# Optimization experiments

Measured on AMD Instinct MI355X. Metric: run time of the kernel, lower is better.

## Reference

```python
import jax, jax.numpy as jnp
import numpy as np

B, S, D, H = 4, 2048, 1024, 16
HD = D // H  # head_size = 64


def setup_inputs() -> dict:
    key = jax.random.key(0)
    kx, kq, kk, kv = jax.random.split(key, 4)
    scale = 1.0 / np.sqrt(D)
    return {
        "x": jax.random.normal(kx, (B, S, D), dtype=jnp.float32),
        "Wq": jax.random.normal(kq, (H, HD, D), dtype=jnp.float32) * scale,
        "Wk": jax.random.normal(kk, (H, HD, D), dtype=jnp.float32) * scale,
        "Wv": jax.random.normal(kv, (H, HD, D), dtype=jnp.float32) * scale,
    }


def reference(x, Wq, Wk, Wv):
    # Per-head projections (Linear with weight [out, in]: y = x @ W.T),
    # vectorized over heads: [B,S,D] x [H,HD,D] -> [B,H,S,HD]
    q = jnp.einsum('bsd,hed->bhse', x, Wq)
    k = jnp.einsum('bsd,hed->bhse', x, Wk)
    v = jnp.einsum('bsd,hed->bhse', x, Wv)

    # Scaled scores: [B,H,S,S]
    att = jnp.einsum('bhqe,bhke->bhqk', q, k) / jnp.sqrt(jnp.asarray(HD, x.dtype))

    # Causal mask (lower-triangular incl. diagonal)
    causal = jnp.tril(jnp.ones((S, S), dtype=bool))
    att = jnp.where(causal, att, -jnp.inf)
    att = jax.nn.softmax(att, axis=-1)

    # Weighted values, then concat heads along feature dim -> [B,S,D]
    out = jnp.einsum('bhqk,bhke->bhqe', att, v)
    out = out.transpose(0, 2, 1, 3).reshape(B, S, H * HD)
    return out
```

## Files before the change

kernel.cpp:

```cpp
#include <hip/hip_runtime.h>
#include <hip/hip_bf16.h>

#define BATCH 4
#define S_LEN 2048
#define D_DIM 1024
#define NHEAD 16
#define HDIM 64

#define QSCALE 0.18033688011112042f

typedef __attribute__((ext_vector_type(8))) __bf16 bf16x8;
typedef __attribute__((ext_vector_type(4))) __bf16 bf16x4;
typedef __attribute__((ext_vector_type(4))) float f32x4;
typedef __attribute__((ext_vector_type(16))) float f32x16;

static __device__ inline unsigned int bf16_bits(float f) {
    __bf16 h = (__bf16)f;
    return (unsigned int)__builtin_bit_cast(unsigned short, h);
}
static __device__ inline unsigned int pkbf(float a, float b) {
    return bf16_bits(a) | (bf16_bits(b) << 16);
}

#define NX8 1048576
#define NW8 131072

__global__ __launch_bounds__(256) void cvt_all_kernel(
    const float* __restrict__ x,  const float* __restrict__ Wq,
    const float* __restrict__ Wk, const float* __restrict__ Wv,
    __bf16* __restrict__ xb, __bf16* __restrict__ wcat)
{
    const int i = blockIdx.x * 256 + threadIdx.x;
    const float* src;
    __bf16* dst;
    if (i < NX8) {
        src = x + (size_t)i * 8;
        dst = xb + (size_t)i * 8;
    } else {
        const int i2 = i - NX8;
        const int w  = i2 >> 17;
        src = ((w == 0) ? Wq : (w == 1) ? Wk : Wv) + (size_t)(i2 & (NW8 - 1)) * 8;
        dst = wcat + (size_t)i2 * 8;
    }
    const f32x4* p = reinterpret_cast<const f32x4*>(src);
    f32x4 a = p[0], b = p[1];
    bf16x8 r;
    r[0] = (__bf16)a[0]; r[1] = (__bf16)a[1]; r[2] = (__bf16)a[2]; r[3] = (__bf16)a[3];
    r[4] = (__bf16)b[0]; r[5] = (__bf16)b[1]; r[6] = (__bf16)b[2]; r[7] = (__bf16)b[3];
    *reinterpret_cast<bf16x8*>(dst) = r;
}

__global__ __launch_bounds__(256) void proj_gemm_kernel(
    const __bf16* __restrict__ xb, const __bf16* __restrict__ wb,
    __bf16* __restrict__ qo, __bf16* __restrict__ ko, __bf16* __restrict__ vto)
{
    __shared__ __bf16 As[128][32];
    __shared__ __bf16 Bs[128][32];

    const int tid = threadIdx.x;
    const int l  = tid & 63;
    const int w  = tid >> 6;
    const int wm = w >> 1, wn = w & 1;
    const int lr = l & 15, lg = l >> 4, lk = lg * 8;
    const int m0 = blockIdx.y * 128;
    const int n0 = blockIdx.x * 128;
    const int mat = n0 >> 10;
    const int nb  = n0 & 1023;

    const int sr = l >> 2;
    const int sc = (l & 3) * 8;
    const int g0 = w * 2;

    f32x4 acc[4][4] = {};

    for (int d = 0; d < D_DIM; d += 32) {
        __builtin_amdgcn_global_load_lds(
            (const __attribute__((address_space(1))) void*)(xb + (size_t)(m0 + g0 * 16 + sr) * D_DIM + d + sc),
            (__attribute__((address_space(3))) void*)(&As[g0 * 16][0]), 16, 0, 0);
        __builtin_amdgcn_global_load_lds(
            (const __attribute__((address_space(1))) void*)(xb + (size_t)(m0 + (g0 + 1) * 16 + sr) * D_DIM + d + sc),
            (__attribute__((address_space(3))) void*)(&As[(g0 + 1) * 16][0]), 16, 0, 0);
        __builtin_amdgcn_global_load_lds(
            (const __attribute__((address_space(1))) void*)(wb + (size_t)(n0 + g0 * 16 + sr) * D_DIM + d + sc),
            (__attribute__((address_space(3))) void*)(&Bs[g0 * 16][0]), 16, 0, 0);
        __builtin_amdgcn_global_load_lds(
            (const __attribute__((address_space(1))) void*)(wb + (size_t)(n0 + (g0 + 1) * 16 + sr) * D_DIM + d + sc),
            (__attribute__((address_space(3))) void*)(&Bs[(g0 + 1) * 16][0]), 16, 0, 0);
        __syncthreads();

        bf16x8 af[4], bfr[4];
        #pragma unroll
        for (int mi = 0; mi < 4; ++mi)
            af[mi] = *reinterpret_cast<const bf16x8*>(&As[wm * 64 + mi * 16 + lr][lk]);
        #pragma unroll
        for (int ni = 0; ni < 4; ++ni)
            bfr[ni] = *reinterpret_cast<const bf16x8*>(&Bs[wn * 64 + ni * 16 + lr][lk]);
        #pragma unroll
        for (int mi = 0; mi < 4; ++mi) {
            #pragma unroll
            for (int ni = 0; ni < 4; ++ni)
                acc[mi][ni] = __builtin_amdgcn_mfma_f32_16x16x32_bf16(
                    af[mi], bfr[ni], acc[mi][ni], 0, 0, 0);
        }
        __syncthreads();
    }

    const float oscale = (mat == 0) ? QSCALE : 1.0f;
    #pragma unroll
    for (int mi = 0; mi < 4; ++mi) {
        const int mrow = m0 + wm * 64 + mi * 16 + lg * 4;
        const int b = mrow >> 11;
        const int s = mrow & (S_LEN - 1);
        #pragma unroll
        for (int ni = 0; ni < 4; ++ni) {
            const int n = nb + wn * 64 + ni * 16 + lr;
            const int h = n >> 6;
            const int e = n & 63;
            if (mat == 2) {
                bf16x4 pk;
                #pragma unroll
                for (int r = 0; r < 4; ++r) pk[r] = (__bf16)acc[mi][ni][r];
                *reinterpret_cast<bf16x4*>(
                    vto + ((size_t)(b * NHEAD + h) * HDIM + e) * S_LEN + s) = pk;
            } else {
                __bf16* __restrict__ dst = (mat == 0) ? qo : ko;
                #pragma unroll
                for (int r = 0; r < 4; ++r)
                    dst[((size_t)(b * NHEAD + h) * S_LEN + (s + r)) * HDIM + e] =
                        (__bf16)(acc[mi][ni][r] * oscale);
            }
        }
    }
}

template<int T, bool MASK>
__device__ __attribute__((always_inline)) inline void sm_pack(
    int kv0, int qbase, int lq, int lh,
    f32x16& s0, f32x16& s1,
    float (&m_acc)[2], float (&l_lane)[2], f32x16 (&acc)[2][2],
    bf16x8 (&pB)[4])
{
    if (MASK) {
        const int qrow = qbase + T * 32 + lq;
        #pragma unroll
        for (int r = 0; r < 16; ++r) {
            const int kvl = (r & 3) + 8 * (r >> 2) + 4 * lh;
            if (kv0 + kvl > qrow)      s0[r] = -1e30f;
            if (kv0 + 32 + kvl > qrow) s1[r] = -1e30f;
        }
    }

    float tm[8];
    #pragma unroll
    for (int r = 0; r < 8; ++r)
        tm[r] = fmaxf(fmaxf(s0[r], s0[r + 8]), fmaxf(s1[r], s1[r + 8]));
    float mx = fmaxf(fmaxf(fmaxf(tm[0], tm[1]), fmaxf(tm[2], tm[3])),
                     fmaxf(fmaxf(tm[4], tm[5]), fmaxf(tm[6], tm[7])));

    if (!__all(mx - m_acc[T] <= 8.0f)) {
        mx = fmaxf(mx, __shfl_xor(mx, 32));
        const float mnew = fmaxf(m_acc[T], mx);
        const float sc = exp2f(m_acc[T] - mnew);
        l_lane[T] *= sc;
        acc[T][0] *= sc;
        acc[T][1] *= sc;
        m_acc[T] = mnew;
    }

    const float mt = m_acc[T];
    float p0[16], p1[16];
    float psum = 0.0f;
    #pragma unroll
    for (int r = 0; r < 16; ++r) { p0[r] = exp2f(s0[r] - mt); psum += p0[r]; }
    #pragma unroll
    for (int r = 0; r < 16; ++r) { p1[r] = exp2f(s1[r] - mt); psum += p1[r]; }
    l_lane[T] += psum;

    #pragma unroll
    for (int sl = 0; sl < 2; ++sl) {
        const int b = sl * 8;
        {
            unsigned A = pkbf(p0[b + 0], p0[b + 1]);
            unsigned C = pkbf(p0[b + 2], p0[b + 3]);
            unsigned B = pkbf(p0[b + 4], p0[b + 5]);
            unsigned D = pkbf(p0[b + 6], p0[b + 7]);
            auto r0 = __builtin_amdgcn_permlane32_swap((int)A, (int)B, false, false);
            auto r1 = __builtin_amdgcn_permlane32_swap((int)C, (int)D, false, false);
            uint4 u;
            u.x = (unsigned)r0[0]; u.y = (unsigned)r1[0];
            u.z = (unsigned)r0[1]; u.w = (unsigned)r1[1];
            pB[sl] = __builtin_bit_cast(bf16x8, u);
        }
        {
            unsigned A = pkbf(p1[b + 0], p1[b + 1]);
            unsigned C = pkbf(p1[b + 2], p1[b + 3]);
            unsigned B = pkbf(p1[b + 4], p1[b + 5]);
            unsigned D = pkbf(p1[b + 6], p1[b + 7]);
            auto r0 = __builtin_amdgcn_permlane32_swap((int)A, (int)B, false, false);
            auto r1 = __builtin_amdgcn_permlane32_swap((int)C, (int)D, false, false);
            uint4 u;
            u.x = (unsigned)r0[0]; u.y = (unsigned)r1[0];
            u.z = (unsigned)r0[1]; u.w = (unsigned)r1[1];
            pB[2 + sl] = __builtin_bit_cast(bf16x8, u);
        }
    }
}

template<bool MASK>
__device__ __attribute__((always_inline)) inline void pair_compute(
    int kv0, int qbase, int lq, int lh,
    const __bf16* __restrict__ kp, const __bf16* __restrict__ vp,
    const bf16x8 (&qB)[2][4],
    float (&m_acc)[2], float (&l_lane)[2], f32x16 (&acc)[2][2])
{
    const int kcol = 8 * lh;

    bf16x8 kA[2][4];
    #pragma unroll
    for (int kvb = 0; kvb < 2; ++kvb)
        #pragma unroll
        for (int ks = 0; ks < 4; ++ks)
            kA[kvb][ks] = *reinterpret_cast<const bf16x8*>(
                kp + (size_t)(kv0 + kvb * 32 + lq) * HDIM + ks * 16 + kcol);

    f32x16 s00 = {}, s01 = {}, s10 = {}, s11 = {};
    __builtin_amdgcn_s_setprio(1);
    #pragma unroll
    for (int ks = 0; ks < 4; ++ks)
        s00 = __builtin_amdgcn_mfma_f32_32x32x16_bf16(kA[0][ks], qB[0][ks], s00, 0, 0, 0);
    #pragma unroll
    for (int ks = 0; ks < 4; ++ks)
        s01 = __builtin_amdgcn_mfma_f32_32x32x16_bf16(kA[1][ks], qB[0][ks], s01, 0, 0, 0);
    #pragma unroll
    for (int ks = 0; ks < 4; ++ks)
        s10 = __builtin_amdgcn_mfma_f32_32x32x16_bf16(kA[0][ks], qB[1][ks], s10, 0, 0, 0);
    #pragma unroll
    for (int ks = 0; ks < 4; ++ks)
        s11 = __builtin_amdgcn_mfma_f32_32x32x16_bf16(kA[1][ks], qB[1][ks], s11, 0, 0, 0);
    __builtin_amdgcn_s_setprio(0);

    bf16x8 vA[2][4];
    #pragma unroll
    for (int eb = 0; eb < 2; ++eb)
        #pragma unroll
        for (int ks = 0; ks < 4; ++ks)
            vA[eb][ks] = *reinterpret_cast<const bf16x8*>(
                vp + (size_t)(eb * 32 + lq) * S_LEN + kv0 + ks * 16 + kcol);

    bf16x8 pB0[4];
    sm_pack<0, MASK>(kv0, qbase, lq, lh, s00, s01, m_acc, l_lane, acc, pB0);

    __builtin_amdgcn_s_setprio(1);
    #pragma unroll
    for (int eb = 0; eb < 2; ++eb)
        #pragma unroll
        for (int ks = 0; ks < 4; ++ks)
            acc[0][eb] = __builtin_amdgcn_mfma_f32_32x32x16_bf16(
                vA[eb][ks], pB0[ks], acc[0][eb], 0, 0, 0);
    __builtin_amdgcn_s_setprio(0);

    bf16x8 pB1[4];
    sm_pack<1, MASK>(kv0, qbase, lq, lh, s10, s11, m_acc, l_lane, acc, pB1);

    __builtin_amdgcn_s_setprio(1);
    #pragma unroll
    for (int eb = 0; eb < 2; ++eb)
        #pragma unroll
        for (int ks = 0; ks < 4; ++ks)
            acc[1][eb] = __builtin_amdgcn_mfma_f32_32x32x16_bf16(
                vA[eb][ks], pB1[ks], acc[1][eb], 0, 0, 0);
    __builtin_amdgcn_s_setprio(0);
}

template<int T>
__device__ __attribute__((always_inline)) inline void expose_tile(
    float* region, int l, const float (&m_acc)[2], const float (&lt)[2],
    const f32x16 (&acc)[2][2])
{
    float* p = region + l * 35;
    p[0] = m_acc[T];
    p[1] = lt[T];
    #pragma unroll
    for (int eb = 0; eb < 2; ++eb)
        #pragma unroll
        for (int r = 0; r < 16; ++r)
            p[2 + eb * 16 + r] = acc[T][eb][r];
}

template<int T>
__device__ __attribute__((always_inline)) inline void merge_out(
    const float* region, int l, int lh, const float (&m_acc)[2],
    const float (&lt)[2], const f32x16 (&acc)[2][2], float* orow)
{
    const float* p = region + l * 35;
    const float mo = p[0];
    const float lo = p[1];
    const float mn = fmaxf(m_acc[T], mo);
    const float s_own = exp2f(m_acc[T] - mn);
    const float s_oth = exp2f(mo - mn);
    const float liv = 1.0f / (lt[T] * s_own + lo * s_oth);
    #pragma unroll
    for (int eb = 0; eb < 2; ++eb) {
        #pragma unroll
        for (int g = 0; g < 4; ++g) {
            f32x4 ox;
            #pragma unroll
            for (int r = 0; r < 4; ++r) {
                const float oth = p[2 + eb * 16 + g * 4 + r];
                ox[r] = (acc[T][eb][g * 4 + r] * s_own + oth * s_oth) * liv;
            }
            *reinterpret_cast<f32x4*>(orow + eb * 32 + g * 8 + 4 * lh) = ox;
        }
    }
}

__global__ __launch_bounds__(128, 2) void attn_kernel(
    const __bf16* __restrict__ q, const __bf16* __restrict__ k,
    const __bf16* __restrict__ vt, float* __restrict__ out)
{
    __shared__ float mlds[2 * 64 * 35];

    const int tid = threadIdx.x;
    const int l  = tid & 63;
    const int w  = tid >> 6;
    const int lq = l & 31;
    const int lh = l >> 5;
    const int kcol = 8 * lh;

    const int n   = blockIdx.x;
    const int xcd = n & 7;
    const int m   = n >> 3;
    const int tp  = m >> 3;
    const int bh  = xcd * 8 + (m & 7);

    const __bf16* __restrict__ kp = k  + (size_t)bh * S_LEN * HDIM;
    const __bf16* __restrict__ vp = vt + (size_t)bh * HDIM * S_LEN;
    const int bq = bh >> 4;
    const int hq = bh & 15;

    #pragma unroll 1
    for (int ph = 0; ph < 2; ++ph) {
        const int qq    = ph ? (31 - tp) : tp;
        const int qbase = qq * 64;
        const int nkv   = qq + 1;

        const __bf16* __restrict__ qp = q + ((size_t)bh * S_LEN + qbase) * HDIM;
        bf16x8 qB[2][4];
        #pragma unroll
        for (int t = 0; t < 2; ++t)
            #pragma unroll
            for (int ks = 0; ks < 4; ++ks)
                qB[t][ks] = *reinterpret_cast<const bf16x8*>(
                    qp + (size_t)(t * 32 + lq) * HDIM + ks * 16 + kcol);

        float m_acc[2], l_lane[2];
        f32x16 acc[2][2] = {};
        #pragma unroll
        for (int t = 0; t < 2; ++t) { m_acc[t] = -1e30f; l_lane[t] = 0.0f; }

        #pragma unroll 1
        for (int j = w; j < nkv - 1; j += 2)
            pair_compute<false>(j * 64, qbase, lq, lh, kp, vp,
                                qB, m_acc, l_lane, acc);
        if (((nkv - 1) & 1) == w)
            pair_compute<true>((nkv - 1) * 64, qbase, lq, lh, kp, vp,
                               qB, m_acc, l_lane, acc);

        float lt[2];
        lt[0] = l_lane[0] + __shfl_xor(l_lane[0], 32);
        lt[1] = l_lane[1] + __shfl_xor(l_lane[1], 32);

        float* myreg = mlds + w * (64 * 35);
        if (w == 0) expose_tile<1>(myreg, l, m_acc, lt, acc);
        else        expose_tile<0>(myreg, l, m_acc, lt, acc);
        __syncthreads();

        const float* other = mlds + (1 - w) * (64 * 35);
        if (w == 0) {
            float* orow = out + (size_t)(bq * S_LEN + qbase + 0 * 32 + lq) * D_DIM + hq * HDIM;
            merge_out<0>(other, l, lh, m_acc, lt, acc, orow);
        } else {
            float* orow = out + (size_t)(bq * S_LEN + qbase + 1 * 32 + lq) * D_DIM + hq * HDIM;
            merge_out<1>(other, l, lh, m_acc, lt, acc, orow);
        }
        __syncthreads();
    }
}

extern "C" void kernel_launch(void* const* d_in, const int* in_sizes, int n_in,
                              void* d_out, int out_size, void* d_ws, size_t ws_size,
                              hipStream_t stream)
{
    const float* x  = (const float*)d_in[0];
    const float* Wq = (const float*)d_in[1];
    const float* Wk = (const float*)d_in[2];
    const float* Wv = (const float*)d_in[3];
    float* out = (float*)d_out;

    const size_t x_elems = (size_t)BATCH * S_LEN * D_DIM;
    __bf16* xb   = (__bf16*)d_out;
    __bf16* wcat = xb + x_elems;

    const size_t per_buf = (size_t)BATCH * NHEAD * S_LEN * HDIM;
    __bf16* qb = (__bf16*)d_ws;
    __bf16* kb = qb + per_buf;
    __bf16* vb = kb + per_buf;

    cvt_all_kernel<<<dim3((NX8 + 3 * NW8) / 256), dim3(256), 0, stream>>>(
        x, Wq, Wk, Wv, xb, wcat);

    dim3 grid1(3 * D_DIM / 128, (BATCH * S_LEN) / 128);
    proj_gemm_kernel<<<grid1, dim3(256), 0, stream>>>(xb, wcat, qb, kb, vb);

    attn_kernel<<<dim3(1024), dim3(128), 0, stream>>>(qb, kb, vb, out);
}
```

Before: 156.9 us.

## Stage K and V tiles into swizzled LDS via global_load_lds

Instead of each wave loading its K and V fragments straight from global memory into registers, the block now stages two 64-row K tiles and two V tiles into LDS with direct global-to-LDS loads. Wave 0 loads the K tiles and wave 1 loads the V tiles, and both waves then read their fragments from LDS using an XOR swizzle to avoid bank conflicts. The goal is coalesced, asynchronous global traffic and less register-side latency. The cost is two block barriers per step with no double buffering, so load latency is no longer overlapped with MFMA work. LDS use also grows to 32 KB, which may limit occupancy.

Measured after the change: 161.5 us. +3.0%, slower.

```diff
diff --git a/kernel.cpp b/kernel.cpp
--- a/kernel.cpp
+++ b/kernel.cpp
@@ -133,6 +133,22 @@
     }
 }
 
+__device__ __attribute__((always_inline)) inline void stage_tile(
+    __bf16* dst, const __bf16* __restrict__ src_base, size_t row_stride,
+    int col0, int l)
+{
+    const int r8   = l >> 3;
+    const int csw  = ((l & 7) ^ r8) * 8;
+    #pragma unroll
+    for (int i = 0; i < 8; ++i) {
+        __builtin_amdgcn_global_load_lds(
+            (const __attribute__((address_space(1))) void*)(
+                src_base + (size_t)(i * 8 + r8) * row_stride + col0 + csw),
+            (__attribute__((address_space(3))) void*)(dst + i * 512),
+            16, 0, 0);
+    }
+}
+
 template<int T, bool MASK>
 __device__ __attribute__((always_inline)) inline void sm_pack(
     int kv0, int qbase, int lq, int lh,
@@ -209,19 +225,20 @@
 template<bool MASK>
 __device__ __attribute__((always_inline)) inline void pair_compute(
     int kv0, int qbase, int lq, int lh,
-    const __bf16* __restrict__ kp, const __bf16* __restrict__ vp,
+    const __bf16* __restrict__ kt, const __bf16* __restrict__ vt,
     const bf16x8 (&qB)[2][4],
     float (&m_acc)[2], float (&l_lane)[2], f32x16 (&acc)[2][2])
 {
-    const int kcol = 8 * lh;
-
     bf16x8 kA[2][4];
     #pragma unroll
-    for (int kvb = 0; kvb < 2; ++kvb)
+    for (int kvb = 0; kvb < 2; ++kvb) {
+        const int row = kvb * 32 + lq;
+        const int sw  = row & 7;
         #pragma unroll
         for (int ks = 0; ks < 4; ++ks)
             kA[kvb][ks] = *reinterpret_cast<const bf16x8*>(
-                kp + (size_t)(kv0 + kvb * 32 + lq) * HDIM + ks * 16 + kcol);
+                kt + row * 64 + ((ks * 2 + lh) ^ sw) * 8);
+    }
 
     f32x16 s00 = {}, s01 = {}, s10 = {}, s11 = {};
     __builtin_amdgcn_s_setprio(1);
@@ -241,11 +258,14 @@
 
     bf16x8 vA[2][4];
     #pragma unroll
-    for (int eb = 0; eb < 2; ++eb)
+    for (int eb = 0; eb < 2; ++eb) {
+        const int row = eb * 32 + lq;
+        const int sw  = row & 7;
         #pragma unroll
         for (int ks = 0; ks < 4; ++ks)
             vA[eb][ks] = *reinterpret_cast<const bf16x8*>(
-                vp + (size_t)(eb * 32 + lq) * S_LEN + kv0 + ks * 16 + kcol);
+                vt + row * 64 + ((ks * 2 + lh) ^ sw) * 8);
+    }
 
     bf16x8 pB0[4];
     sm_pack<0, MASK>(kv0, qbase, lq, lh, s00, s01, m_acc, l_lane, acc, pB0);
@@ -318,14 +338,13 @@
     const __bf16* __restrict__ q, const __bf16* __restrict__ k,
     const __bf16* __restrict__ vt, float* __restrict__ out)
 {
-    __shared__ float mlds[2 * 64 * 35];
+    __shared__ __align__(16) unsigned char smem[32768];
 
     const int tid = threadIdx.x;
     const int l  = tid & 63;
     const int w  = tid >> 6;
     const int lq = l & 31;
     const int lh = l >> 5;
-    const int kcol = 8 * lh;
 
     const int n   = blockIdx.x;
     const int xcd = n & 7;
@@ -338,12 +357,18 @@
     const int bq = bh >> 4;
     const int hq = bh & 15;
 
+    __bf16* klds0 = reinterpret_cast<__bf16*>(smem);
+    __bf16* klds1 = klds0 + 4096;
+    __bf16* vlds0 = klds1 + 4096;
+    __bf16* vlds1 = vlds0 + 4096;
+
     #pragma unroll 1
     for (int ph = 0; ph < 2; ++ph) {
         const int qq    = ph ? (31 - tp) : tp;
         const int qbase = qq * 64;
         const int nkv   = qq + 1;
 
+        const int kcol = 8 * lh;
         const __bf16* __restrict__ qp = q + ((size_t)bh * S_LEN + qbase) * HDIM;
         bf16x8 qB[2][4];
         #pragma unroll
@@ -358,24 +383,45 @@
         #pragma unroll
         for (int t = 0; t < 2; ++t) { m_acc[t] = -1e30f; l_lane[t] = 0.0f; }
 
+        const int ns = (nkv + 1) >> 1;
         #pragma unroll 1
-        for (int j = w; j < nkv - 1; j += 2)
-            pair_compute<false>(j * 64, qbase, lq, lh, kp, vp,
-                                qB, m_acc, l_lane, acc);
-        if (((nkv - 1) & 1) == w)
-            pair_compute<true>((nkv - 1) * 64, qbase, lq, lh, kp, vp,
-                               qB, m_acc, l_lane, acc);
+        for (int s = 0; s < ns; ++s) {
+            const int j0 = 2 * s;
+            const int j1 = 2 * s + 1;
+            if (w == 0) {
+                stage_tile(klds0, kp + (size_t)j0 * 64 * HDIM, HDIM, 0, l);
+                if (j1 < nkv) stage_tile(klds1, kp + (size_t)j1 * 64 * HDIM, HDIM, 0, l);
+            } else {
+                stage_tile(vlds0, vp, S_LEN, j0 * 64, l);
+                if (j1 < nkv) stage_tile(vlds1, vp, S_LEN, j1 * 64, l);
+            }
+            __syncthreads();
+
+            const int j = j0 + w;
+            if (j < nkv) {
+                const __bf16* kt = (w == 0) ? klds0 : klds1;
+                const __bf16* vl = (w == 0) ? vlds0 : vlds1;
+                if (j == nkv - 1)
+                    pair_compute<true>(j * 64, qbase, lq, lh, kt, vl,
+                                       qB, m_acc, l_lane, acc);
+                else
+                    pair_compute<false>(j * 64, qbase, lq, lh, kt, vl,
+                                        qB, m_acc, l_lane, acc);
+            }
+            __syncthreads();
+        }
 
         float lt[2];
         lt[0] = l_lane[0] + __shfl_xor(l_lane[0], 32);
         lt[1] = l_lane[1] + __shfl_xor(l_lane[1], 32);
 
-        float* myreg = mlds + w * (64 * 35);
+        float* mbase = reinterpret_cast<float*>(smem);
+        float* myreg = mbase + w * (64 * 35);
         if (w == 0) expose_tile<1>(myreg, l, m_acc, lt, acc);
         else        expose_tile<0>(myreg, l, m_acc, lt, acc);
         __syncthreads();
 
-        const float* other = mlds + (1 - w) * (64 * 35);
+        const float* other = mbase + (1 - w) * (64 * 35);
         if (w == 0) {
             float* orow = out + (size_t)(bq * S_LEN + qbase + 0 * 32 + lq) * D_DIM + hq * HDIM;
             merge_out<0>(other, l, lh, m_acc, lt, acc, orow);
```
